# Kernel optimization log

Hardware: AMD Instinct MI355X
Metric: run time of the kernel (lower is better)

The kernel has to match this reference:

```python
import jax, jax.numpy as jnp
import numpy as np

MEM_LEN = 1024
EPS = 1e-5


def _layer_norm(x, g, b):
    mu = jnp.mean(x, axis=-1, keepdims=True)
    var = jnp.mean((x - mu) ** 2, axis=-1, keepdims=True)
    return (x - mu) * jax.lax.rsqrt(var + EPS) * g + b


def _rel_shift(t):
    # t: [B, H, T, L] -> TXL pad->view->slice->view shift
    B, H, T, L = t.shape
    padded = jnp.concatenate([jnp.zeros((B, H, T, 1), t.dtype), t], axis=-1)
    padded = padded.reshape(B, H, L + 1, T)
    return padded[:, :, 1:, :].reshape(B, H, T, L)


def _pos_emb(length, d_model, dtype):
    inv_freq = 1.0 / (10000.0 ** (np.arange(0, d_model, 2, dtype=np.float32) / d_model))
    pos_seq = np.arange(length - 1, -1, -1, dtype=np.float32)
    sin_inp = np.outer(pos_seq, inv_freq)
    pe = np.concatenate([np.sin(sin_inp), np.cos(sin_inp)], axis=-1)
    return jnp.asarray(pe, dtype=dtype)


def setup_inputs() -> dict:
    key = jax.random.key(0)
    ks = jax.random.split(key, 12)
    B, T, M, D, H, Dff = 4, 1024, 1024, 1024, 16, 4096
    dh = D // H
    s = 1.0 / np.sqrt(D)
    return {
        "x": jax.random.normal(ks[0], (B, T, D), jnp.float32),
        "mem": jax.random.normal(ks[1], (B, M, D), jnp.float32),
        "Wq": jax.random.normal(ks[2], (D, D), jnp.float32) * s,
        "Wk": jax.random.normal(ks[3], (D, D), jnp.float32) * s,
        "Wv": jax.random.normal(ks[4], (D, D), jnp.float32) * s,
        "Wr": jax.random.normal(ks[5], (D, D), jnp.float32) * s,
        "Wo": jax.random.normal(ks[6], (D, D), jnp.float32) * s,
        "bias_u": jax.random.normal(ks[7], (H, dh), jnp.float32) * 0.02,
        "bias_v": jax.random.normal(ks[8], (H, dh), jnp.float32) * 0.02,
        "ln1_g": jnp.ones((D,), jnp.float32),
        "ln1_b": jnp.zeros((D,), jnp.float32),
        "ln2_g": jnp.ones((D,), jnp.float32),
        "ln2_b": jnp.zeros((D,), jnp.float32),
        "W1": jax.random.normal(ks[9], (D, Dff), jnp.float32) * s,
        "b1": jnp.zeros((Dff,), jnp.float32),
        "W2": jax.random.normal(ks[10], (Dff, D), jnp.float32) * (1.0 / np.sqrt(Dff)),
        "b2": jnp.zeros((D,), jnp.float32),
    }


def reference(x, mem, Wq, Wk, Wv, Wr, Wo, bias_u, bias_v,
              ln1_g, ln1_b, ln2_g, ln2_b, W1, b1, W2, b2):
    B, T, D = x.shape
    M = mem.shape[1]
    H, dh = bias_u.shape
    L = T + M
    scale = 1.0 / np.sqrt(dh)

    residual = x
    xn = _layer_norm(x, ln1_g, ln1_b)

    cat = jnp.concatenate([mem_n := mem, xn], axis=1) if False else jnp.concatenate([mem, xn], axis=1)
    # NOTE: torch concatenates raw memory states (not re-normalized) with norm_x.
    k = (cat @ Wk).reshape(B, L, H, dh).transpose(0, 2, 1, 3)      # [B,H,L,dh]
    v = (cat @ Wv).reshape(B, L, H, dh).transpose(0, 2, 1, 3)      # [B,H,L,dh]
    q = (xn @ Wq).reshape(B, T, H, dh).transpose(0, 2, 1, 3)       # [B,H,T,dh]

    pe = _pos_emb(L, D, x.dtype)                                   # [L,D]
    r = (pe @ Wr).reshape(L, H, dh).transpose(1, 0, 2)             # [H,L,dh]

    content = jnp.einsum("bhid,bhjd->bhij", q + bias_u[None, :, None, :], k)
    rel = jnp.einsum("bhid,hjd->bhij", q + bias_v[None, :, None, :], r)
    rel = _rel_shift(rel)

    attn = jax.nn.softmax((content + rel) * scale, axis=-1)        # [B,H,T,L]
    out = jnp.einsum("bhij,bhjd->bhid", attn, v)                   # [B,H,T,dh]
    out = out.transpose(0, 2, 1, 3).reshape(B, T, D) @ Wo

    x2 = residual + out
    xf = _layer_norm(x2, ln2_g, ln2_b)
    ff = jax.nn.gelu(xf @ W1 + b1, approximate=False) @ W2 + b2
    y = x2 + ff

    new_mem = jax.lax.stop_gradient(
        jnp.concatenate([mem, residual], axis=1)[:, -MEM_LEN:])
    return y, new_mem
```

## Files before the change

kernel.cpp:

```cpp
#include <hip/hip_runtime.h>
#include <hip/hip_bf16.h>

typedef short bf16x8 __attribute__((ext_vector_type(8)));
typedef float f32x4 __attribute__((ext_vector_type(4)));
typedef unsigned short u16;

__device__ __forceinline__ float bf2f(u16 u) {
    union { unsigned int i; float f; } x; x.i = ((unsigned int)u) << 16; return x.f;
}
__device__ __forceinline__ u16 f2bf(float f) {
    union { float f; unsigned int i; } x; x.f = f;
    unsigned int r = x.i + 0x7fff + ((x.i >> 16) & 1);
    return (u16)(r >> 16);
}
__device__ __forceinline__ f32x4 mfma16(bf16x8 a, bf16x8 b, f32x4 c) {
    return __builtin_amdgcn_mfma_f32_16x16x32_bf16(a, b, c, 0, 0, 0);
}
#define GLL16(lds_base, gsrc) \
    __builtin_amdgcn_global_load_lds((const __attribute__((address_space(1))) void*)(gsrc), \
                                     (__attribute__((address_space(3))) void*)(lds_base), 16, 0, 0)

__global__ __launch_bounds__(256)
void transpose5_kernel(const float* __restrict__ s0, const float* __restrict__ s1,
                       const float* __restrict__ s2, const float* __restrict__ s3,
                       const float* __restrict__ s4,
                       u16* __restrict__ d0, u16* __restrict__ d1,
                       u16* __restrict__ d2, u16* __restrict__ d3,
                       u16* __restrict__ d4) {
    const float* in; u16* out;
    switch (blockIdx.z) {
        case 0: in = s0; out = d0; break;
        case 1: in = s1; out = d1; break;
        case 2: in = s2; out = d2; break;
        case 3: in = s3; out = d3; break;
        default: in = s4; out = d4; break;
    }
    __shared__ float t[32][33];
    const int c0 = blockIdx.x * 32, r0 = blockIdx.y * 32;
    const int tx = threadIdx.x & 31, ty = threadIdx.x >> 5;
#pragma unroll
    for (int i = 0; i < 32; i += 8) t[ty + i][tx] = in[(size_t)(r0 + ty + i) * 1024 + c0 + tx];
    __syncthreads();
#pragma unroll
    for (int i = 0; i < 32; i += 8) out[(size_t)(c0 + ty + i) * 1024 + r0 + tx] = f2bf(t[tx][ty + i]);
}

__global__ __launch_bounds__(256)
void transpose_kernel(const float* __restrict__ in, u16* __restrict__ out, int R, int C) {
    __shared__ float t[32][33];
    const int c0 = blockIdx.x * 32, r0 = blockIdx.y * 32;
    const int tx = threadIdx.x & 31, ty = threadIdx.x >> 5;
#pragma unroll
    for (int i = 0; i < 32; i += 8) t[ty + i][tx] = in[(size_t)(r0 + ty + i) * C + c0 + tx];
    __syncthreads();
#pragma unroll
    for (int i = 0; i < 32; i += 8) out[(size_t)(c0 + ty + i) * R + r0 + tx] = f2bf(t[tx][ty + i]);
}

__global__ __launch_bounds__(256)
void convert_kernel(const float* __restrict__ in, u16* __restrict__ out) {
    const size_t i = ((size_t)blockIdx.x * 256 + threadIdx.x) * 8;
    const float4 a = *(const float4*)(in + i);
    const float4 b = *(const float4*)(in + i + 4);
    bf16x8 o;
    o[0] = (short)f2bf(a.x); o[1] = (short)f2bf(a.y);
    o[2] = (short)f2bf(a.z); o[3] = (short)f2bf(a.w);
    o[4] = (short)f2bf(b.x); o[5] = (short)f2bf(b.y);
    o[6] = (short)f2bf(b.z); o[7] = (short)f2bf(b.w);
    *(bf16x8*)(out + i) = o;
}

__global__ __launch_bounds__(256)
void pe_kernel(u16* __restrict__ pe) {
    const int idx = blockIdx.x * 256 + threadIdx.x;
    const int p = idx >> 10, d = idx & 1023;
    const float pos = (float)(2047 - p);
    const int k = d & 511;
    const float invf = powf(10000.f, ((float)(2 * k)) * (-1.f / 1024.f));
    const float a = pos * invf;
    pe[idx] = f2bf((d < 512) ? sinf(a) : cosf(a));
}

__global__ __launch_bounds__(256)
void ln_kernel(const float* __restrict__ inp, const float* __restrict__ gg,
               const float* __restrict__ bb, u16* __restrict__ outp) {
    const int row = blockIdx.x * 4 + (threadIdx.x >> 6);
    const int l = threadIdx.x & 63;
    const size_t base = (size_t)row * 1024 + l * 16;
    float v[16];
    const float4* p4 = (const float4*)(inp + base);
#pragma unroll
    for (int j = 0; j < 4; ++j) {
        float4 f = p4[j];
        v[j*4+0] = f.x; v[j*4+1] = f.y; v[j*4+2] = f.z; v[j*4+3] = f.w;
    }
    float s = 0.f, s2 = 0.f;
#pragma unroll
    for (int j = 0; j < 16; ++j) { s += v[j]; s2 += v[j] * v[j]; }
#pragma unroll
    for (int off = 1; off < 64; off <<= 1) {
        s += __shfl_xor(s, off, 64);
        s2 += __shfl_xor(s2, off, 64);
    }
    const float mu = s * 0.0009765625f;
    const float var = s2 * 0.0009765625f - mu * mu;
    const float rs = rsqrtf(var + 1e-5f);
#pragma unroll
    for (int j = 0; j < 16; ++j)
        outp[base + j] = f2bf((v[j] - mu) * rs * gg[l * 16 + j] + bb[l * 16 + j]);
}

template<int EPI, bool CATA>
__global__ __launch_bounds__(256)
void gemm_kernel(const u16* __restrict__ A, const u16* __restrict__ A2,
                 const u16* __restrict__ Wt, void* __restrict__ outp,
                 u16* __restrict__ out2, const float* __restrict__ cb1,
                 const float* __restrict__ cb2, const float* __restrict__ residp,
                 int Mdim, int Ndim, int Kdim) {
    __shared__ __attribute__((aligned(16))) u16 As[128 * 32];
    __shared__ __attribute__((aligned(16))) u16 Bs[128 * 32];
    const int tid = threadIdx.x;
    const int w = tid >> 6, l = tid & 63;
    const int wr = w >> 1, wc = w & 1;
    const int m0 = blockIdx.x * 128, n0 = blockIdx.y * 128;
    f32x4 acc[4][4] = {};

    for (int k0 = 0; k0 < Kdim; k0 += 32) {
        __syncthreads();
#pragma unroll
        for (int p = 0; p < 2; ++p) {
            const int ebase = (p * 4 + w) * 512;
            const int e = ebase + l * 8;
            const int row = e >> 5, colk = e & 31;
            const u16* srcA;
            if (CATA) {
                const int rr = m0 + row;
                const int bb_ = rr >> 11, pos = rr & 2047;
                srcA = (pos < 1024 ? A + ((size_t)(bb_ * 1024 + pos)) * 1024
                                   : A2 + ((size_t)(bb_ * 1024 + pos - 1024)) * 1024)
                       + (k0 + colk);
            } else {
                srcA = A + (size_t)(m0 + row) * Kdim + (k0 + colk);
            }
            const u16* srcB = Wt + (size_t)(n0 + row) * Kdim + (k0 + colk);
            GLL16(&As[ebase], srcA);
            GLL16(&Bs[ebase], srcB);
        }
        __syncthreads();
        bf16x8 af[4], bfr[4];
#pragma unroll
        for (int mi = 0; mi < 4; ++mi)
            af[mi] = *(const bf16x8*)&As[(wr * 64 + mi * 16 + (l & 15)) * 32 + (l >> 4) * 8];
#pragma unroll
        for (int ni = 0; ni < 4; ++ni)
            bfr[ni] = *(const bf16x8*)&Bs[(wc * 64 + ni * 16 + (l & 15)) * 32 + (l >> 4) * 8];
#pragma unroll
        for (int mi = 0; mi < 4; ++mi)
#pragma unroll
            for (int ni = 0; ni < 4; ++ni)
                acc[mi][ni] = mfma16(af[mi], bfr[ni], acc[mi][ni]);
    }

#pragma unroll
    for (int mi = 0; mi < 4; ++mi)
#pragma unroll
        for (int ni = 0; ni < 4; ++ni)
#pragma unroll
            for (int rg = 0; rg < 4; ++rg) {
                const int row = m0 + wr * 64 + mi * 16 + (l >> 4) * 4 + rg;
                const int col = n0 + wc * 64 + ni * 16 + (l & 15);
                const size_t idx = (size_t)row * Ndim + col;
                const float v = acc[mi][ni][rg];
                if (EPI == 0) {
                    ((u16*)outp)[idx] = f2bf(v);
                } else if (EPI == 1) {
                    ((u16*)outp)[idx] = f2bf(v + cb1[col]);
                    out2[idx] = f2bf(v + cb2[col]);
                } else if (EPI == 2) {
                    ((float*)outp)[idx] = v + residp[idx];
                } else if (EPI == 3) {
                    const float t = v + cb1[col];
                    ((u16*)outp)[idx] = f2bf(0.5f * t * (1.f + erff(t * 0.70710678118654752f)));
                } else {
                    ((float*)outp)[idx] = v + cb1[col] + residp[idx];
                }
            }
}

template<int EPI>
__global__ __launch_bounds__(256)
void gemm64_kernel(const u16* __restrict__ A, const u16* __restrict__ Wt,
                   void* __restrict__ outp, u16* __restrict__ out2,
                   const float* __restrict__ cb1, const float* __restrict__ cb2,
                   const float* __restrict__ residp,
                   int Mdim, int Ndim, int Kdim) {
    __shared__ __attribute__((aligned(16))) u16 As[64 * 32];
    __shared__ __attribute__((aligned(16))) u16 Bs[128 * 32];
    const int tid = threadIdx.x;
    const int w = tid >> 6, l = tid & 63;
    const int m0 = blockIdx.x * 64, n0 = blockIdx.y * 128;
    f32x4 acc[4][2] = {};

    for (int k0 = 0; k0 < Kdim; k0 += 32) {
        __syncthreads();
        {
            const int e = (w * 64 + l) * 8;
            const int row = e >> 5, colk = e & 31;
            GLL16(&As[w * 512], A + (size_t)(m0 + row) * Kdim + (k0 + colk));
        }
#pragma unroll
        for (int p = 0; p < 2; ++p) {
            const int ebase = (p * 4 + w) * 512;
            const int e = ebase + l * 8;
            const int row = e >> 5, colk = e & 31;
            GLL16(&Bs[ebase], Wt + (size_t)(n0 + row) * Kdim + (k0 + colk));
        }
        __syncthreads();
        bf16x8 af[4], bfr[2];
#pragma unroll
        for (int mi = 0; mi < 4; ++mi)
            af[mi] = *(const bf16x8*)&As[(mi * 16 + (l & 15)) * 32 + (l >> 4) * 8];
#pragma unroll
        for (int ni = 0; ni < 2; ++ni)
            bfr[ni] = *(const bf16x8*)&Bs[(w * 32 + ni * 16 + (l & 15)) * 32 + (l >> 4) * 8];
#pragma unroll
        for (int mi = 0; mi < 4; ++mi)
#pragma unroll
            for (int ni = 0; ni < 2; ++ni)
                acc[mi][ni] = mfma16(af[mi], bfr[ni], acc[mi][ni]);
    }

#pragma unroll
    for (int mi = 0; mi < 4; ++mi)
#pragma unroll
        for (int ni = 0; ni < 2; ++ni)
#pragma unroll
            for (int rg = 0; rg < 4; ++rg) {
                const int row = m0 + mi * 16 + (l >> 4) * 4 + rg;
                const int col = n0 + w * 32 + ni * 16 + (l & 15);
                const size_t idx = (size_t)row * Ndim + col;
                const float v = acc[mi][ni][rg];
                if (EPI == 0) {
                    ((u16*)outp)[idx] = f2bf(v);
                } else if (EPI == 1) {
                    ((u16*)outp)[idx] = f2bf(v + cb1[col]);
                    out2[idx] = f2bf(v + cb2[col]);
                } else if (EPI == 2) {
                    ((float*)outp)[idx] = v + residp[idx];
                } else {
                    ((float*)outp)[idx] = v + cb1[col] + residp[idx];
                }
            }
}

__global__ __launch_bounds__(256)
void gemm_kv_kernel(const u16* __restrict__ A, const u16* __restrict__ A2,
                    const u16* __restrict__ WtK, const u16* __restrict__ WtV,
                    u16* __restrict__ outK, u16* __restrict__ outV) {
    __shared__ __attribute__((aligned(16))) u16 As[128 * 32];
    __shared__ __attribute__((aligned(16))) u16 Bk[128 * 32];
    __shared__ __attribute__((aligned(16))) u16 Bv[128 * 32];
    const int tid = threadIdx.x;
    const int w = tid >> 6, l = tid & 63;
    const int wr = w >> 1, wc = w & 1;
    const int m0 = blockIdx.x * 128, n0 = blockIdx.y * 128;
    f32x4 acck[4][4] = {};
    f32x4 accv[4][4] = {};

    for (int k0 = 0; k0 < 1024; k0 += 32) {
        __syncthreads();
#pragma unroll
        for (int p = 0; p < 2; ++p) {
            const int ebase = (p * 4 + w) * 512;
            const int e = ebase + l * 8;
            const int row = e >> 5, colk = e & 31;
            const int rr = m0 + row;
            const int bb_ = rr >> 11, pos = rr & 2047;
            const u16* srcA = (pos < 1024 ? A + ((size_t)(bb_ * 1024 + pos)) * 1024
                                          : A2 + ((size_t)(bb_ * 1024 + pos - 1024)) * 1024)
                              + (k0 + colk);
            GLL16(&As[ebase], srcA);
            GLL16(&Bk[ebase], WtK + (size_t)(n0 + row) * 1024 + (k0 + colk));
            GLL16(&Bv[ebase], WtV + (size_t)(n0 + row) * 1024 + (k0 + colk));
        }
        __syncthreads();
        bf16x8 af[4], bkf[4], bvf[4];
#pragma unroll
        for (int mi = 0; mi < 4; ++mi)
            af[mi] = *(const bf16x8*)&As[(wr * 64 + mi * 16 + (l & 15)) * 32 + (l >> 4) * 8];
#pragma unroll
        for (int ni = 0; ni < 4; ++ni) {
            const int off = (wc * 64 + ni * 16 + (l & 15)) * 32 + (l >> 4) * 8;
            bkf[ni] = *(const bf16x8*)&Bk[off];
            bvf[ni] = *(const bf16x8*)&Bv[off];
        }
#pragma unroll
        for (int mi = 0; mi < 4; ++mi)
#pragma unroll
            for (int ni = 0; ni < 4; ++ni) {
                acck[mi][ni] = mfma16(af[mi], bkf[ni], acck[mi][ni]);
                accv[mi][ni] = mfma16(af[mi], bvf[ni], accv[mi][ni]);
            }
    }

#pragma unroll
    for (int mi = 0; mi < 4; ++mi)
#pragma unroll
        for (int ni = 0; ni < 4; ++ni)
#pragma unroll
            for (int rg = 0; rg < 4; ++rg) {
                const int row = m0 + wr * 64 + mi * 16 + (l >> 4) * 4 + rg;
                const int col = n0 + wc * 64 + ni * 16 + (l & 15);
                const size_t idx = (size_t)row * 1024 + col;
                outK[idx] = f2bf(acck[mi][ni][rg]);
                outV[idx] = f2bf(accv[mi][ni][rg]);
            }
}

__global__ __launch_bounds__(256, 2)
void attn_kernel(const u16* __restrict__ qu, const u16* __restrict__ qv,
                 const u16* __restrict__ kcat, const u16* __restrict__ vcat,
                 const u16* __restrict__ rbuf, u16* __restrict__ outp) {
    constexpr int T = 1024, L = 2048, MM = 1024;
    __shared__ __attribute__((aligned(16))) u16 KtL[64 * 64];
    __shared__ __attribute__((aligned(16))) u16 RmL[128 * 64];
    __shared__ __attribute__((aligned(16))) u16 RwL[128 * 64];
    __shared__ __attribute__((aligned(16))) u16 Vt[64][72];
    __shared__ __attribute__((aligned(16))) u16 Pl[4][16][72];
    const int bid = blockIdx.x;
    const int g = (bid & 7) + 8 * (bid >> 7);
    const int it = (bid >> 3) & 15;
    const int h = g & 15, b = g >> 4;
    const int i0 = it * 64;
    const int tid = threadIdx.x;
    const int w = tid >> 6, l = tid & 63;
    const int lg = l >> 4, ll = l & 15;
    const int iw0 = i0 + w * 16;
    const int l8 = l >> 3;
    const int ssrc = ((l & 7) * 8) ^ (l8 << 3);
    const int sA = (lg * 8) ^ ((ll & 7) << 3);
    const int sB = (lg * 8 + 32) ^ ((ll & 7) << 3);

    bf16x8 quf[2], qvf[2];
    const int qc = h * 64 + lg * 8;
    {
        const size_t qrow = (size_t)(b * T + iw0 + ll);
        quf[0] = *(const bf16x8*)&qu[qrow * 1024 + qc];
        quf[1] = *(const bf16x8*)&qu[qrow * 1024 + qc + 32];
        qvf[0] = *(const bf16x8*)&qv[qrow * 1024 + qc];
        qvf[1] = *(const bf16x8*)&qv[qrow * 1024 + qc + 32];
    }
    const int r2 = iw0 + ll + 1;
    const size_t qrow2 = (size_t)(b * T + (r2 < T ? r2 : T - 1));
    const u16* kb = kcat + (size_t)b * L * 1024 + h * 64;
    const u16* vb = vcat + (size_t)b * L * 1024 + h * 64;
    const u16* rb = rbuf + h * 64;

    f32x4 o_acc[4] = {};
    f32x4 o_sum = {0.f, 0.f, 0.f, 0.f};
    float m_run[4] = {-1e30f, -1e30f, -1e30f, -1e30f};
    const bf16x8 onesb = {(short)0x3F80, (short)0x3F80, (short)0x3F80, (short)0x3F80,
                          (short)0x3F80, (short)0x3F80, (short)0x3F80, (short)0x3F80};
    const int vjq = tid & 15, vdg = tid >> 4;

    for (int jt = 0; jt < 32; ++jt) {
        const int j0 = jt * 64;
        const bool main_blk = (j0 <= MM + i0 + 63);
        const bool wrap_blk = (j0 + 63 >= MM + i0 + 2);
        __syncthreads();
#pragma unroll
        for (int p = 0; p < 2; ++p) {
            const int k8 = w * 2 + p;
            GLL16(&KtL[k8 * 512], kb + (size_t)(j0 + k8 * 8 + l8) * 1024 + ssrc);
        }
        if (main_blk) {
            const long bm = (long)j0 + T - i0 - 64;
#pragma unroll
            for (int p = 0; p < 4; ++p) {
                const int k8 = w * 4 + p;
                GLL16(&RmL[k8 * 512], rb + (long)(bm + k8 * 8 + l8) * 1024 + ssrc);
            }
        }
        if (wrap_blk) {
            const long bw_ = (long)j0 - MM - i0 - 65;
#pragma unroll
            for (int p = 0; p < 4; ++p) {
                const int k8 = w * 4 + p;
                GLL16(&RwL[k8 * 512], rb + (long)(bw_ + k8 * 8 + l8) * 1024 + ssrc);
            }
        }
        {
            const u16* srcv = vb + (size_t)(j0 + vjq) * 1024 + vdg * 4;
            const ushort4 r0 = *(const ushort4*)(srcv);
            const ushort4 r1 = *(const ushort4*)(srcv + 16 * 1024);
            const ushort4 r2w = *(const ushort4*)(srcv + 32 * 1024);
            const ushort4 r3 = *(const ushort4*)(srcv + 48 * 1024);
            const ushort4 c0 = {r0.x, r1.x, r2w.x, r3.x};
            const ushort4 c1 = {r0.y, r1.y, r2w.y, r3.y};
            const ushort4 c2 = {r0.z, r1.z, r2w.z, r3.z};
            const ushort4 c3 = {r0.w, r1.w, r2w.w, r3.w};
            *(ushort4*)&Vt[vdg * 4 + 0][vjq * 4] = c0;
            *(ushort4*)&Vt[vdg * 4 + 1][vjq * 4] = c1;
            *(ushort4*)&Vt[vdg * 4 + 2][vjq * 4] = c2;
            *(ushort4*)&Vt[vdg * 4 + 3][vjq * 4] = c3;
        }
        __syncthreads();

        f32x4 sv[4];
        __builtin_amdgcn_s_setprio(1);
#pragma unroll
        for (int ns = 0; ns < 4; ++ns) {
            const int rowb = (ns * 16 + ll) * 64;
            f32x4 a = {0.f, 0.f, 0.f, 0.f};
            a = mfma16(quf[0], *(const bf16x8*)&KtL[rowb + sA], a);
            a = mfma16(quf[1], *(const bf16x8*)&KtL[rowb + sB], a);
            sv[ns] = a;
        }
        __builtin_amdgcn_s_setprio(0);

        if (j0 <= MM + iw0 + 15) {
            const int trb = 48 - 16 * w;
            f32x4 gb[5];
#pragma unroll
            for (int cs = 0; cs < 5; ++cs) {
                const int rowb = (trb + cs * 16 + ll) * 64;
                f32x4 a = {0.f, 0.f, 0.f, 0.f};
                a = mfma16(qvf[0], *(const bf16x8*)&RmL[rowb + sA], a);
                a = mfma16(qvf[1], *(const bf16x8*)&RmL[rowb + sB], a);
                gb[cs] = a;
            }
#pragma unroll
            for (int r = 0; r < 4; ++r) {
                const int i_loc = lg * 4 + r;
                const int srcl = (l & 48) | ((ll + 15 - i_loc) & 15);
                const float sh0 = __shfl(gb[0][r], srcl, 64);
                const float sh1 = __shfl(gb[1][r], srcl, 64);
                const float sh2 = __shfl(gb[2][r], srcl, 64);
                const float sh3 = __shfl(gb[3][r], srcl, 64);
                const float sh4 = __shfl(gb[4][r], srcl, 64);
                const bool hi = (ll > i_loc);
                const int thr = MM + iw0 + i_loc - j0;
                const float e0 = hi ? sh1 : sh0;
                const float e1 = hi ? sh2 : sh1;
                const float e2 = hi ? sh3 : sh2;
                const float e3 = hi ? sh4 : sh3;
                if (ll <= thr)      sv[0][r] += e0;
                if (16 + ll <= thr) sv[1][r] += e1;
                if (32 + ll <= thr) sv[2][r] += e2;
                if (48 + ll <= thr) sv[3][r] += e3;
            }
        }
        if (j0 + 63 >= MM + iw0 + 2) {
            const bf16x8 qv2f0 = *(const bf16x8*)&qv[qrow2 * 1024 + qc];
            const bf16x8 qv2f1 = *(const bf16x8*)&qv[qrow2 * 1024 + qc + 32];
            const int trb = 48 - 16 * w;
            f32x4 gb[5];
#pragma unroll
            for (int cs = 0; cs < 5; ++cs) {
                const int rowb = (trb + cs * 16 + ll) * 64;
                f32x4 a = {0.f, 0.f, 0.f, 0.f};
                a = mfma16(qv2f0, *(const bf16x8*)&RwL[rowb + sA], a);
                a = mfma16(qv2f1, *(const bf16x8*)&RwL[rowb + sB], a);
                gb[cs] = a;
            }
#pragma unroll
            for (int r = 0; r < 4; ++r) {
                const int i_loc = lg * 4 + r;
                const int srcl = (l & 48) | ((ll + 15 - i_loc) & 15);
                const float sh0 = __shfl(gb[0][r], srcl, 64);
                const float sh1 = __shfl(gb[1][r], srcl, 64);
                const float sh2 = __shfl(gb[2][r], srcl, 64);
                const float sh3 = __shfl(gb[3][r], srcl, 64);
                const float sh4 = __shfl(gb[4][r], srcl, 64);
                const bool hi = (ll > i_loc);
                const int thr2 = MM + iw0 + i_loc - j0 + 2;
                const float e0 = hi ? sh1 : sh0;
                const float e1 = hi ? sh2 : sh1;
                const float e2 = hi ? sh3 : sh2;
                const float e3 = hi ? sh4 : sh3;
                if (ll >= thr2)      sv[0][r] += e0;
                if (16 + ll >= thr2) sv[1][r] += e1;
                if (32 + ll >= thr2) sv[2][r] += e2;
                if (48 + ll >= thr2) sv[3][r] += e3;
            }
        }

#pragma unroll
        for (int r = 0; r < 4; ++r) {
            const int i_loc = lg * 4 + r;
            const float s0 = sv[0][r] * 0.125f, s1 = sv[1][r] * 0.125f;
            const float s2 = sv[2][r] * 0.125f, s3 = sv[3][r] * 0.125f;
            float pm = fmaxf(fmaxf(s0, s1), fmaxf(s2, s3));
            pm = fmaxf(pm, __shfl_xor(pm, 1, 64));
            pm = fmaxf(pm, __shfl_xor(pm, 2, 64));
            pm = fmaxf(pm, __shfl_xor(pm, 4, 64));
            pm = fmaxf(pm, __shfl_xor(pm, 8, 64));
            const float mnew = fmaxf(m_run[r], pm);
            const float alpha = __expf(m_run[r] - mnew);
            const float p0 = __expf(s0 - mnew), p1 = __expf(s1 - mnew);
            const float p2 = __expf(s2 - mnew), p3 = __expf(s3 - mnew);
            const ushort4 pw = {f2bf(p0), f2bf(p1), f2bf(p2), f2bf(p3)};
            *(ushort4*)&Pl[w][i_loc][ll * 4] = pw;
            m_run[r] = mnew;
            o_sum[r] *= alpha;
#pragma unroll
            for (int ns = 0; ns < 4; ++ns) o_acc[ns][r] *= alpha;
        }

        __builtin_amdgcn_s_setprio(1);
        const bf16x8 ap0 = *(const bf16x8*)&Pl[w][ll][lg * 8];
        const bf16x8 ap1 = *(const bf16x8*)&Pl[w][ll][32 + lg * 8];
#pragma unroll
        for (int ns = 0; ns < 4; ++ns) {
            const bf16x8 bv0 = *(const bf16x8*)&Vt[ns * 16 + ll][lg * 8];
            const bf16x8 bv1 = *(const bf16x8*)&Vt[ns * 16 + ll][32 + lg * 8];
            o_acc[ns] = mfma16(ap0, bv0, o_acc[ns]);
            o_acc[ns] = mfma16(ap1, bv1, o_acc[ns]);
        }
        o_sum = mfma16(ap0, onesb, o_sum);
        o_sum = mfma16(ap1, onesb, o_sum);
        __builtin_amdgcn_s_setprio(0);
    }

#pragma unroll
    for (int ns = 0; ns < 4; ++ns)
#pragma unroll
        for (int r = 0; r < 4; ++r) {
            const int row = iw0 + lg * 4 + r;
            outp[(size_t)(b * T + row) * 1024 + h * 64 + ns * 16 + ll] =
                f2bf(o_acc[ns][r] / o_sum[r]);
        }
}

extern "C" void kernel_launch(void* const* d_in, const int* in_sizes, int n_in,
                              void* d_out, int out_size, void* d_ws, size_t ws_size,
                              hipStream_t stream) {
    const float* x    = (const float*)d_in[0];
    const float* mem  = (const float*)d_in[1];
    const float* Wq   = (const float*)d_in[2];
    const float* Wk   = (const float*)d_in[3];
    const float* Wv   = (const float*)d_in[4];
    const float* Wr   = (const float*)d_in[5];
    const float* Wo   = (const float*)d_in[6];
    const float* bu   = (const float*)d_in[7];
    const float* bv   = (const float*)d_in[8];
    const float* ln1g = (const float*)d_in[9];
    const float* ln1b = (const float*)d_in[10];
    const float* ln2g = (const float*)d_in[11];
    const float* ln2b = (const float*)d_in[12];
    const float* W1   = (const float*)d_in[13];
    const float* b1   = (const float*)d_in[14];
    const float* W2   = (const float*)d_in[15];
    const float* b2   = (const float*)d_in[16];

    float* y_out   = (float*)d_out;
    float* mem_out = (float*)d_out + 4194304;

    char* dob = (char*)d_out;
    u16* attno     = (u16*)(dob + 0);
    u16* pe        = (u16*)(dob + (size_t)8  * 1048576);
    u16* rbuf_base = (u16*)(dob + (size_t)12 * 1048576);
    u16* rbuf      = rbuf_base + 80 * 1024;
    char* dw = dob + (size_t)16 * 1048576 + 524288;
    u16* WqT = (u16*)(dw);
    u16* WkT = (u16*)(dw + (size_t)2 * 1048576);
    u16* WvT = (u16*)(dw + (size_t)4 * 1048576);
    u16* WrT = (u16*)(dw + (size_t)6 * 1048576);
    u16* WoT = (u16*)(dw + (size_t)8 * 1048576);

    char* ws = (char*)d_ws;
    const size_t MB = 1u << 20;
    u16*  xn    = (u16*)(ws + 0 * MB);
    u16*  x2n   = (u16*)(ws + 0 * MB);
    u16*  W2T   = (u16*)(ws + 0 * MB);
    u16*  qu    = (u16*)(ws + 8 * MB);
    float* x2f  = (float*)(ws + 8 * MB);
    u16*  qv    = (u16*)(ws + 16 * MB);
    u16*  kcat  = (u16*)(ws + 24 * MB);
    u16*  ffh   = (u16*)(ws + 24 * MB);
    u16*  vcat  = (u16*)(ws + 40 * MB);
    u16*  memb  = (u16*)(ws + 56 * MB);
    u16*  W1T   = (u16*)(ws + 56 * MB);

    transpose5_kernel<<<dim3(32, 32, 5), 256, 0, stream>>>(Wq, Wk, Wv, Wr, Wo,
                                                           WqT, WkT, WvT, WrT, WoT);
    pe_kernel<<<8192, 256, 0, stream>>>(pe);
    convert_kernel<<<2048, 256, 0, stream>>>(mem, memb);
    ln_kernel<<<1024, 256, 0, stream>>>(x, ln1g, ln1b, xn);
    gemm64_kernel<0><<<dim3(32, 8), 256, 0, stream>>>(pe, WrT, rbuf, nullptr, nullptr, nullptr, nullptr, 2048, 1024, 1024);
    gemm64_kernel<1><<<dim3(64, 8), 256, 0, stream>>>(xn, WqT, qu, qv, bu, bv, nullptr, 4096, 1024, 1024);
    gemm_kv_kernel<<<dim3(64, 8), 256, 0, stream>>>(memb, xn, WkT, WvT, kcat, vcat);
    attn_kernel<<<1024, 256, 0, stream>>>(qu, qv, kcat, vcat, rbuf, attno);
    gemm64_kernel<2><<<dim3(64, 8), 256, 0, stream>>>(attno, WoT, x2f, nullptr, nullptr, nullptr, x, 4096, 1024, 1024);
    transpose_kernel<<<dim3(128, 32), 256, 0, stream>>>(W1, W1T, 1024, 4096);
    hipMemcpyAsync(mem_out, x, (size_t)4194304 * 4, hipMemcpyDeviceToDevice, stream);
    ln_kernel<<<1024, 256, 0, stream>>>(x2f, ln2g, ln2b, x2n);
    gemm_kernel<3, false><<<dim3(32, 32), 256, 0, stream>>>(x2n, nullptr, W1T, ffh, nullptr, b1, nullptr, nullptr, 4096, 4096, 1024);
    transpose_kernel<<<dim3(32, 128), 256, 0, stream>>>(W2, W2T, 4096, 1024);
    gemm64_kernel<4><<<dim3(64, 8), 256, 0, stream>>>(ffh, W2T, y_out, nullptr, b2, nullptr, x2f, 4096, 1024, 4096);
    (void)in_sizes; (void)n_in; (void)out_size; (void)ws_size;
}
```

Before: 538.8 us.

## Double-buffer K and V tiles and prefetch next tile during softmax and PV

The attention kernel now keeps two LDS buffers for the K and transposed-V tiles. It issues the loads for the next key block (K, R main/wrap, V into registers) right after the score computation, so memory latency overlaps with the softmax and P·V MFMA work. This costs extra LDS (about 17 KB more per block), which may reduce occupancy at two blocks per CU, plus more live registers for the staged V values. R buffers stay single-buffered, guarded by the barrier that follows score use.

```diff
diff --git a/kernel.cpp b/kernel.cpp
--- a/kernel.cpp
+++ b/kernel.cpp
@@ -322,10 +322,10 @@
                  const u16* __restrict__ kcat, const u16* __restrict__ vcat,
                  const u16* __restrict__ rbuf, u16* __restrict__ outp) {
     constexpr int T = 1024, L = 2048, MM = 1024;
-    __shared__ __attribute__((aligned(16))) u16 KtL[64 * 64];
+    __shared__ __attribute__((aligned(16))) u16 KtL[2][64 * 64];
     __shared__ __attribute__((aligned(16))) u16 RmL[128 * 64];
     __shared__ __attribute__((aligned(16))) u16 RwL[128 * 64];
-    __shared__ __attribute__((aligned(16))) u16 Vt[64][72];
+    __shared__ __attribute__((aligned(16))) u16 Vt[2][64][72];
     __shared__ __attribute__((aligned(16))) u16 Pl[4][16][72];
     const int bid = blockIdx.x;
     const int g = (bid & 7) + 8 * (bid >> 7);
@@ -363,48 +363,35 @@
                           (short)0x3F80, (short)0x3F80, (short)0x3F80, (short)0x3F80};
     const int vjq = tid & 15, vdg = tid >> 4;
 
+#pragma unroll
+    for (int p = 0; p < 2; ++p) {
+        const int k8 = w * 2 + p;
+        GLL16(&KtL[0][k8 * 512], kb + (size_t)(k8 * 8 + l8) * 1024 + ssrc);
+    }
+    {
+        const long bm = (long)T - i0 - 64;
+#pragma unroll
+        for (int p = 0; p < 4; ++p) {
+            const int k8 = w * 4 + p;
+            GLL16(&RmL[k8 * 512], rb + (long)(bm + k8 * 8 + l8) * 1024 + ssrc);
+        }
+        const u16* srcv = vb + (size_t)vjq * 1024 + vdg * 4;
+        const ushort4 r0 = *(const ushort4*)(srcv);
+        const ushort4 r1 = *(const ushort4*)(srcv + 16 * 1024);
+        const ushort4 r2w = *(const ushort4*)(srcv + 32 * 1024);
+        const ushort4 r3 = *(const ushort4*)(srcv + 48 * 1024);
+        *(ushort4*)&Vt[0][vdg * 4 + 0][vjq * 4] = (ushort4){r0.x, r1.x, r2w.x, r3.x};
+        *(ushort4*)&Vt[0][vdg * 4 + 1][vjq * 4] = (ushort4){r0.y, r1.y, r2w.y, r3.y};
+        *(ushort4*)&Vt[0][vdg * 4 + 2][vjq * 4] = (ushort4){r0.z, r1.z, r2w.z, r3.z};
+        *(ushort4*)&Vt[0][vdg * 4 + 3][vjq * 4] = (ushort4){r0.w, r1.w, r2w.w, r3.w};
+    }
+    __syncthreads();
+
     for (int jt = 0; jt < 32; ++jt) {
         const int j0 = jt * 64;
+        const int buf = jt & 1;
         const bool main_blk = (j0 <= MM + i0 + 63);
         const bool wrap_blk = (j0 + 63 >= MM + i0 + 2);
-        __syncthreads();
-#pragma unroll
-        for (int p = 0; p < 2; ++p) {
-            const int k8 = w * 2 + p;
-            GLL16(&KtL[k8 * 512], kb + (size_t)(j0 + k8 * 8 + l8) * 1024 + ssrc);
-        }
-        if (main_blk) {
-            const long bm = (long)j0 + T - i0 - 64;
-#pragma unroll
-            for (int p = 0; p < 4; ++p) {
-                const int k8 = w * 4 + p;
-                GLL16(&RmL[k8 * 512], rb + (long)(bm + k8 * 8 + l8) * 1024 + ssrc);
-            }
-        }
-        if (wrap_blk) {
-            const long bw_ = (long)j0 - MM - i0 - 65;
-#pragma unroll
-            for (int p = 0; p < 4; ++p) {
-                const int k8 = w * 4 + p;
-                GLL16(&RwL[k8 * 512], rb + (long)(bw_ + k8 * 8 + l8) * 1024 + ssrc);
-            }
-        }
-        {
-            const u16* srcv = vb + (size_t)(j0 + vjq) * 1024 + vdg * 4;
-            const ushort4 r0 = *(const ushort4*)(srcv);
-            const ushort4 r1 = *(const ushort4*)(srcv + 16 * 1024);
-            const ushort4 r2w = *(const ushort4*)(srcv + 32 * 1024);
-            const ushort4 r3 = *(const ushort4*)(srcv + 48 * 1024);
-            const ushort4 c0 = {r0.x, r1.x, r2w.x, r3.x};
-            const ushort4 c1 = {r0.y, r1.y, r2w.y, r3.y};
-            const ushort4 c2 = {r0.z, r1.z, r2w.z, r3.z};
-            const ushort4 c3 = {r0.w, r1.w, r2w.w, r3.w};
-            *(ushort4*)&Vt[vdg * 4 + 0][vjq * 4] = c0;
-            *(ushort4*)&Vt[vdg * 4 + 1][vjq * 4] = c1;
-            *(ushort4*)&Vt[vdg * 4 + 2][vjq * 4] = c2;
-            *(ushort4*)&Vt[vdg * 4 + 3][vjq * 4] = c3;
-        }
-        __syncthreads();
 
         f32x4 sv[4];
         __builtin_amdgcn_s_setprio(1);
@@ -412,13 +399,13 @@
         for (int ns = 0; ns < 4; ++ns) {
             const int rowb = (ns * 16 + ll) * 64;
             f32x4 a = {0.f, 0.f, 0.f, 0.f};
-            a = mfma16(quf[0], *(const bf16x8*)&KtL[rowb + sA], a);
-            a = mfma16(quf[1], *(const bf16x8*)&KtL[rowb + sB], a);
+            a = mfma16(quf[0], *(const bf16x8*)&KtL[buf][rowb + sA], a);
+            a = mfma16(quf[1], *(const bf16x8*)&KtL[buf][rowb + sB], a);
             sv[ns] = a;
         }
         __builtin_amdgcn_s_setprio(0);
 
-        if (j0 <= MM + iw0 + 15) {
+        if (main_blk && j0 <= MM + iw0 + 15) {
             const int trb = 48 - 16 * w;
             f32x4 gb[5];
 #pragma unroll
@@ -450,7 +437,7 @@
                 if (48 + ll <= thr) sv[3][r] += e3;
             }
         }
-        if (j0 + 63 >= MM + iw0 + 2) {
+        if (wrap_blk && j0 + 63 >= MM + iw0 + 2) {
             const bf16x8 qv2f0 = *(const bf16x8*)&qv[qrow2 * 1024 + qc];
             const bf16x8 qv2f1 = *(const bf16x8*)&qv[qrow2 * 1024 + qc + 32];
             const int trb = 48 - 16 * w;
@@ -484,6 +471,38 @@
                 if (48 + ll >= thr2) sv[3][r] += e3;
             }
         }
+        __syncthreads();
+
+        ushort4 vr0, vr1, vr2, vr3;
+        if (jt < 31) {
+            const int j1 = j0 + 64;
+#pragma unroll
+            for (int p = 0; p < 2; ++p) {
+                const int k8 = w * 2 + p;
+                GLL16(&KtL[buf ^ 1][k8 * 512], kb + (size_t)(j1 + k8 * 8 + l8) * 1024 + ssrc);
+            }
+            if (j1 <= MM + i0 + 63) {
+                const long bm = (long)j1 + T - i0 - 64;
+#pragma unroll
+                for (int p = 0; p < 4; ++p) {
+                    const int k8 = w * 4 + p;
+                    GLL16(&RmL[k8 * 512], rb + (long)(bm + k8 * 8 + l8) * 1024 + ssrc);
+                }
+            }
+            if (j1 + 63 >= MM + i0 + 2) {
+                const long bw_ = (long)j1 - MM - i0 - 65;
+#pragma unroll
+                for (int p = 0; p < 4; ++p) {
+                    const int k8 = w * 4 + p;
+                    GLL16(&RwL[k8 * 512], rb + (long)(bw_ + k8 * 8 + l8) * 1024 + ssrc);
+                }
+            }
+            const u16* srcv = vb + (size_t)(j1 + vjq) * 1024 + vdg * 4;
+            vr0 = *(const ushort4*)(srcv);
+            vr1 = *(const ushort4*)(srcv + 16 * 1024);
+            vr2 = *(const ushort4*)(srcv + 32 * 1024);
+            vr3 = *(const ushort4*)(srcv + 48 * 1024);
+        }
 
 #pragma unroll
         for (int r = 0; r < 4; ++r) {
@@ -512,14 +531,22 @@
         const bf16x8 ap1 = *(const bf16x8*)&Pl[w][ll][32 + lg * 8];
 #pragma unroll
         for (int ns = 0; ns < 4; ++ns) {
-            const bf16x8 bv0 = *(const bf16x8*)&Vt[ns * 16 + ll][lg * 8];
-            const bf16x8 bv1 = *(const bf16x8*)&Vt[ns * 16 + ll][32 + lg * 8];
+            const bf16x8 bv0 = *(const bf16x8*)&Vt[buf][ns * 16 + ll][lg * 8];
+            const bf16x8 bv1 = *(const bf16x8*)&Vt[buf][ns * 16 + ll][32 + lg * 8];
             o_acc[ns] = mfma16(ap0, bv0, o_acc[ns]);
             o_acc[ns] = mfma16(ap1, bv1, o_acc[ns]);
         }
         o_sum = mfma16(ap0, onesb, o_sum);
         o_sum = mfma16(ap1, onesb, o_sum);
         __builtin_amdgcn_s_setprio(0);
+
+        if (jt < 31) {
+            *(ushort4*)&Vt[buf ^ 1][vdg * 4 + 0][vjq * 4] = (ushort4){vr0.x, vr1.x, vr2.x, vr3.x};
+            *(ushort4*)&Vt[buf ^ 1][vdg * 4 + 1][vjq * 4] = (ushort4){vr0.y, vr1.y, vr2.y, vr3.y};
+            *(ushort4*)&Vt[buf ^ 1][vdg * 4 + 2][vjq * 4] = (ushort4){vr0.z, vr1.z, vr2.z, vr3.z};
+            *(ushort4*)&Vt[buf ^ 1][vdg * 4 + 3][vjq * 4] = (ushort4){vr0.w, vr1.w, vr2.w, vr3.w};
+        }
+        __syncthreads();
     }
 
 #pragma unroll
```

Measured after the change: 539.6 us. No clear change (+0.2%).
